# Kernel tuning notes

Hardware: AMD Instinct MI355X
Metric: run time of the kernel (lower is better)

The kernel has to match this reference:

```python
import jax, jax.numpy as jnp
import numpy as np

V, N = 3, 32768
C2, C3 = 256, 32          # feat_ch_2D, feat_ch_3D
H = W = 128               # 2D feature map size
D = 32                    # 3D volume feature size
CIN = C2 + C3             # 288, MLP in_channels


def setup_inputs() -> dict:
    key = jax.random.key(0)
    ks = jax.random.split(key, 16)
    sc = 0.02
    inp = {
        'pts': jax.random.uniform(ks[0], (1, N, 3), minval=-0.5, maxval=0.5),
        'pts_proj': jax.random.uniform(ks[1], (1, N, 2), minval=-1.0, maxval=1.0),
        'img_feat0': jax.random.normal(ks[2], (V, C2, H, W)),
        'img_feat1': jax.random.normal(ks[3], (V, C2, H, W)),
        'vol_feat0': jax.random.normal(ks[4], (V, C3, D, D, D)),
        'vol_feat1': jax.random.normal(ks[5], (V, C3, D, D, D)),
        'W0': jax.random.normal(ks[6], (1024, CIN)) * sc,  'b0': jnp.zeros((1024,)),
        'W1': jax.random.normal(ks[7], (512, CIN + 1024)) * sc, 'b1': jnp.zeros((512,)),
        'W2': jax.random.normal(ks[8], (256, CIN + 512)) * sc,  'b2': jnp.zeros((256,)),
        'W3': jax.random.normal(ks[9], (128, CIN + 256)) * sc,  'b3': jnp.zeros((128,)),
        'W4': jax.random.normal(ks[10], (1, 128)) * sc,         'b4': jnp.zeros((1,)),
        'mean_num': 3,
    }
    return inp


def _gs2d(feat, gx, gy):
    # feat: [C,H,W]; gx,gy: [N] normalized coords in [-1,1]
    C, Hh, Ww = feat.shape
    ix = jnp.clip(((gx + 1.0) * Ww - 1.0) * 0.5, 0.0, Ww - 1.0)  # align_corners=False, border pad
    iy = jnp.clip(((gy + 1.0) * Hh - 1.0) * 0.5, 0.0, Hh - 1.0)
    x0f, y0f = jnp.floor(ix), jnp.floor(iy)
    wx, wy = ix - x0f, iy - y0f
    x0 = x0f.astype(jnp.int32); x1 = jnp.minimum(x0 + 1, Ww - 1)
    y0 = y0f.astype(jnp.int32); y1 = jnp.minimum(y0 + 1, Hh - 1)
    v00 = feat[:, y0, x0]; v01 = feat[:, y0, x1]
    v10 = feat[:, y1, x0]; v11 = feat[:, y1, x1]
    return (v00 * (1 - wy) * (1 - wx) + v01 * (1 - wy) * wx
            + v10 * wy * (1 - wx) + v11 * wy * wx)  # [C,N]


def _gs3d(feat, gx, gy, gz):
    # feat: [C,D,H,W]; grid x->W, y->H, z->D (torch grid_sample convention)
    C, Dd, Hh, Ww = feat.shape
    ix = jnp.clip(((gx + 1.0) * Ww - 1.0) * 0.5, 0.0, Ww - 1.0)
    iy = jnp.clip(((gy + 1.0) * Hh - 1.0) * 0.5, 0.0, Hh - 1.0)
    iz = jnp.clip(((gz + 1.0) * Dd - 1.0) * 0.5, 0.0, Dd - 1.0)
    x0f, y0f, z0f = jnp.floor(ix), jnp.floor(iy), jnp.floor(iz)
    wx, wy, wz = ix - x0f, iy - y0f, iz - z0f
    x0 = x0f.astype(jnp.int32); x1 = jnp.minimum(x0 + 1, Ww - 1)
    y0 = y0f.astype(jnp.int32); y1 = jnp.minimum(y0 + 1, Hh - 1)
    z0 = z0f.astype(jnp.int32); z1 = jnp.minimum(z0 + 1, Dd - 1)
    def g(zi, yi, xi):
        return feat[:, zi, yi, xi]  # [C,N]
    out = (g(z0, y0, x0) * (1 - wz) * (1 - wy) * (1 - wx)
           + g(z0, y0, x1) * (1 - wz) * (1 - wy) * wx
           + g(z0, y1, x0) * (1 - wz) * wy * (1 - wx)
           + g(z0, y1, x1) * (1 - wz) * wy * wx
           + g(z1, y0, x0) * wz * (1 - wy) * (1 - wx)
           + g(z1, y0, x1) * wz * (1 - wy) * wx
           + g(z1, y1, x0) * wz * wy * (1 - wx)
           + g(z1, y1, x1) * wz * wy * wx)
    return out  # [C,N]


def _lrelu(x):
    return jnp.where(x >= 0, x, 0.2 * x)


def _conv1x1(Wm, bm, x):
    # x: [V,C,N] -> [V,O,N]
    return jnp.einsum('oc,vcn->von', Wm, x) + bm[None, :, None]


def _mlp0(x, W0, b0, W1, b1, W2, b2, W3, b3):
    out = _lrelu(_conv1x1(W0, b0, x))
    out = _lrelu(_conv1x1(W1, b1, jnp.concatenate([x, out], axis=1)))
    out = _lrelu(_conv1x1(W2, b2, jnp.concatenate([x, out], axis=1)))
    out = _lrelu(_conv1x1(W3, b3, jnp.concatenate([x, out], axis=1)))
    return out  # [V,128,N]


def _forward(pts, pts_proj, img_feats, vol_feats,
             W0, b0, W1, b1, W2, b2, W3, b3, W4, b4, mean_num):
    v = img_feats[0].shape[0]
    gx2 = jnp.broadcast_to(pts_proj[:, :, 0], (v, pts_proj.shape[1]))
    gy2 = jnp.broadcast_to(pts_proj[:, :, 1], (v, pts_proj.shape[1]))
    p = pts * 2.0  # pts *= 2.0 before 3D sampling
    gx3 = jnp.broadcast_to(p[:, :, 0], (v, p.shape[1]))
    gy3 = jnp.broadcast_to(p[:, :, 1], (v, p.shape[1]))
    gz3 = jnp.broadcast_to(p[:, :, 2], (v, p.shape[1]))
    outs = []
    for img_feat, vol_feat in zip(img_feats, vol_feats):
        f2 = jax.vmap(_gs2d)(img_feat, gx2, gy2)            # [V,C2,N]
        f3 = jax.vmap(_gs3d)(vol_feat, gx3, gy3, gz3)       # [V,C3,N]
        pt_feat = jnp.concatenate([f2, f3], axis=1)         # [V,288,N]
        pt_out0 = _mlp0(pt_feat, W0, b0, W1, b1, W2, b2, W3, b3)
        pt_out0_mean = jnp.mean(pt_out0[:mean_num], axis=0, keepdims=True)  # [1,128,N]
        sdf = jax.nn.sigmoid(_conv1x1(W4, b4, pt_out0_mean))                # [1,1,N]
        outs.append(jnp.transpose(sdf, (0, 2, 1)))                          # [1,N,1]
    return tuple(outs)


def reference(pts, pts_proj, img_feat0, img_feat1, vol_feat0, vol_feat1,
              W0, b0, W1, b1, W2, b2, W3, b3, W4, b4, mean_num):
    return _forward(pts, pts_proj, [img_feat0, img_feat1], [vol_feat0, vol_feat1],
                    W0, b0, W1, b1, W2, b2, W3, b3, W4, b4, mean_num)
```

## Files before the change

### kernel.cpp

```cpp
#include <hip/hip_runtime.h>
#include <hip/hip_bf16.h>

#define NV 3
#define NPTS 32768
#define C2C 256
#define C3C 32
#define CINC 288
#define CINP 320
#define HH 128
#define WWW 128
#define DDD 32

typedef short bh8 __attribute__((ext_vector_type(8)));
typedef float fx4 __attribute__((ext_vector_type(4)));
typedef unsigned short us4 __attribute__((ext_vector_type(4)));

__device__ __forceinline__ float b2f(unsigned short u) {
    unsigned int x = ((unsigned int)u) << 16;
    return __uint_as_float(x);
}
__device__ __forceinline__ unsigned short f2b(float f) {
    unsigned int x = __float_as_uint(f);
    unsigned int r = (x + 0x7FFFu + ((x >> 16) & 1u)) >> 16;
    return (unsigned short)r;
}

__device__ __forceinline__ void gl2lds16(const unsigned short* g, unsigned short* l) {
    __builtin_amdgcn_global_load_lds(
        (const __attribute__((address_space(1))) unsigned int*)g,
        (__attribute__((address_space(3))) unsigned int*)l, 16, 0, 0);
}

__device__ __forceinline__ int xcd_swz(int orig, int nwg) {
    int xcd = orig & 7;
    int q = nwg >> 3, r = nwg & 7;
    int base = (xcd < r) ? xcd * (q + 1) : r * (q + 1) + (xcd - r) * q;
    return base + (orig >> 3);
}

__global__ void k_wpad4(const float* __restrict__ s0, const float* __restrict__ s1,
                        const float* __restrict__ s2, const float* __restrict__ s3,
                        unsigned short* __restrict__ d0, unsigned short* __restrict__ d1,
                        unsigned short* __restrict__ d2, unsigned short* __restrict__ d3) {
    const int Ms[4] = {1024, 512, 256, 128};
    const int Kps[4] = {320, 1344, 832, 576};
    int i = blockIdx.y;
    int M = Ms[i], Kp = Kps[i];
    int idx = blockIdx.x * 256 + threadIdx.x;
    if (idx >= M * Kp) return;
    const float* src = (i == 0) ? s0 : (i == 1) ? s1 : (i == 2) ? s2 : s3;
    unsigned short* dst = (i == 0) ? d0 : (i == 1) ? d1 : (i == 2) ? d2 : d3;
    int m = idx / Kp, k = idx - m * Kp;
    int Ksrc = Kp - 32;
    float v;
    if (k < CINC) v = src[(size_t)m * Ksrc + k];
    else if (k < CINP) v = 0.0f;
    else v = src[(size_t)m * Ksrc + (k - 32)];
    dst[idx] = f2b(v);
}

__global__ void k_timg(const float* __restrict__ in0, const float* __restrict__ in1,
                       unsigned short* __restrict__ out, size_t lvlStride) {
    int lvl = blockIdx.z >> 2, cb = blockIdx.z & 3;
    const float* in = lvl ? in1 : in0;
    int v = blockIdx.x >> 7, y = blockIdx.x & 127;
    int x0 = blockIdx.y << 6, c0 = cb << 6;
    __shared__ float t[64][65];
    int tx = threadIdx.x & 63, tg = threadIdx.x >> 6;
    const float* src = in + (((size_t)(v * C2C + c0) * HH + y) * WWW + x0);
#pragma unroll
    for (int i = 0; i < 16; i++) {
        int cl = tg * 16 + i;
        t[cl][tx] = src[(size_t)cl * (HH * WWW) + tx];
    }
    __syncthreads();
    unsigned short* dst = out + lvl * lvlStride + ((size_t)(v * HH + y) * WWW + x0) * C2C + c0;
#pragma unroll
    for (int i = 0; i < 16; i++) {
        int xl = tg * 16 + i;
        dst[(size_t)xl * C2C + tx] = f2b(t[tx][xl]);
    }
}

__global__ void k_tvol(const float* __restrict__ in0, const float* __restrict__ in1,
                       unsigned short* __restrict__ out, size_t lvlStride) {
    int lvl = blockIdx.z;
    const float* in = lvl ? in1 : in0;
    int v = blockIdx.x;
    int s0 = blockIdx.y << 8;
    __shared__ float t[32][257];
    int tid = threadIdx.x;
    const float* src = in + (size_t)v * C3C * 32768 + s0;
#pragma unroll
    for (int c = 0; c < 32; c++) t[c][tid] = src[(size_t)c * 32768 + tid];
    __syncthreads();
    unsigned short* dst = out + lvl * lvlStride + ((size_t)v * 32768 + s0) * C3C;
    int c = tid & 31, sb = tid >> 5;
#pragma unroll
    for (int j = 0; j < 32; j++) {
        int sl = j * 8 + sb;
        dst[(size_t)sl * C3C + c] = f2b(t[c][sl]);
    }
}

__global__ __launch_bounds__(256) void k_sample(const float* __restrict__ pts, const float* __restrict__ proj,
                         const unsigned short* __restrict__ imgT, const unsigned short* __restrict__ volT,
                         unsigned short* __restrict__ ptT, int n0, int Nk) {
    int w = threadIdx.x >> 6, l = threadIdx.x & 63;
    int i = blockIdx.x * 4 + w;
    int v = blockIdx.y;
    int n = n0 + i;
    unsigned short* dstRow = ptT + (size_t)(v * Nk + i) * CINP;

    {
        float gx = proj[n * 2 + 0], gy = proj[n * 2 + 1];
        float ix = fminf(fmaxf(((gx + 1.0f) * (float)WWW - 1.0f) * 0.5f, 0.0f), (float)(WWW - 1));
        float iy = fminf(fmaxf(((gy + 1.0f) * (float)HH - 1.0f) * 0.5f, 0.0f), (float)(HH - 1));
        float x0f = floorf(ix), y0f = floorf(iy);
        float wx = ix - x0f, wy = iy - y0f;
        int x0 = (int)x0f, y0 = (int)y0f;
        int x1 = min(x0 + 1, WWW - 1), y1 = min(y0 + 1, HH - 1);
        const unsigned short* base = imgT + (size_t)v * HH * WWW * C2C;
        us4 a = *((const us4*)(base + ((size_t)(y0 * WWW + x0)) * C2C) + l);
        us4 b = *((const us4*)(base + ((size_t)(y0 * WWW + x1)) * C2C) + l);
        us4 c = *((const us4*)(base + ((size_t)(y1 * WWW + x0)) * C2C) + l);
        us4 d = *((const us4*)(base + ((size_t)(y1 * WWW + x1)) * C2C) + l);
        float w00 = (1.0f - wy) * (1.0f - wx), w01 = (1.0f - wy) * wx;
        float w10 = wy * (1.0f - wx), w11 = wy * wx;
        us4 rv;
#pragma unroll
        for (int r = 0; r < 4; r++) {
            float f = b2f(a[r]) * w00 + b2f(b[r]) * w01 + b2f(c[r]) * w10 + b2f(d[r]) * w11;
            rv[r] = f2b(f);
        }
        *(us4*)(dstRow + l * 4) = rv;
    }
    {
        float gx = pts[n * 3 + 0] * 2.0f, gy = pts[n * 3 + 1] * 2.0f, gz = pts[n * 3 + 2] * 2.0f;
        float ix = fminf(fmaxf(((gx + 1.0f) * (float)DDD - 1.0f) * 0.5f, 0.0f), (float)(DDD - 1));
        float iy = fminf(fmaxf(((gy + 1.0f) * (float)DDD - 1.0f) * 0.5f, 0.0f), (float)(DDD - 1));
        float iz = fminf(fmaxf(((gz + 1.0f) * (float)DDD - 1.0f) * 0.5f, 0.0f), (float)(DDD - 1));
        float x0f = floorf(ix), y0f = floorf(iy), z0f = floorf(iz);
        float wx = ix - x0f, wy = iy - y0f, wz = iz - z0f;
        int x0 = (int)x0f, y0 = (int)y0f, z0 = (int)z0f;
        int x1 = min(x0 + 1, DDD - 1), y1 = min(y0 + 1, DDD - 1), z1 = min(z0 + 1, DDD - 1);
        int c = l & 31, zs = l >> 5;
        int zi = zs ? z1 : z0;
        float wzs = zs ? wz : (1.0f - wz);
        const unsigned short* base = volT + (size_t)v * 32768 * C3C;
        float f00 = b2f(base[((size_t)((zi * 32 + y0) * 32 + x0)) * C3C + c]);
        float f01 = b2f(base[((size_t)((zi * 32 + y0) * 32 + x1)) * C3C + c]);
        float f10 = b2f(base[((size_t)((zi * 32 + y1) * 32 + x0)) * C3C + c]);
        float f11 = b2f(base[((size_t)((zi * 32 + y1) * 32 + x1)) * C3C + c]);
        float r = (f00 * (1.0f - wy) * (1.0f - wx) + f01 * (1.0f - wy) * wx +
                   f10 * wy * (1.0f - wx) + f11 * wy * wx) * wzs;
        float other = __shfl_xor(r, 32);
        r += other;
        if (zs == 0) dstRow[C2C + c] = f2b(r);
    }
    if (l < 8) *(us4*)(dstRow + CINC + l * 4) = (us4){0, 0, 0, 0};
}

template <int K2, int M>
__device__ __forceinline__ void gemm128_body(const unsigned short* __restrict__ A,
                                             const unsigned short* __restrict__ B1,
                                             const unsigned short* __restrict__ B2,
                                             const float* __restrict__ bias,
                                             unsigned short* __restrict__ C) {
    constexpr int K1 = CINP;
    constexpr int K = K1 + K2;
    constexpr int nt1 = K1 / 32;
    constexpr int nt = K / 32;
    __shared__ unsigned short Ash[2][128 * 32];
    __shared__ unsigned short Bsh[2][128 * 32];
    int tid = threadIdx.x;
    int w = tid >> 6, l = tid & 63;
    int la = l & 15, lg = l >> 4;
    int wm = w & 1, wn = w >> 1;
    int gx = gridDim.x;
    int nwg = gx * gridDim.y;
    int bid = xcd_swz(blockIdx.y * gx + blockIdx.x, nwg);
    int mBlk = (bid % gx) * 128;
    int nBlk = (bid / gx) * 128;
    int sRow = l >> 2, sCol = (l & 3) * 8;
    int r0 = w * 32 + sRow, r1 = r0 + 16;

    const unsigned short* Ag = A + (size_t)mBlk * K;
    const unsigned short* B1g = B1 + (size_t)nBlk * K1;
    const unsigned short* B2g = (K2 > 0) ? (B2 + (size_t)nBlk * K2) : (const unsigned short*)0;

    fx4 acc[4][4];
#pragma unroll
    for (int mi = 0; mi < 4; mi++)
#pragma unroll
        for (int ni = 0; ni < 4; ni++) acc[mi][ni] = (fx4){0.f, 0.f, 0.f, 0.f};

    auto stage = [&](int t, int nxt) {
        const unsigned short* as = Ag + t * 32 + sCol;
        gl2lds16(as + (size_t)r0 * K, &Ash[nxt][r0 * 32 + sCol]);
        gl2lds16(as + (size_t)r1 * K, &Ash[nxt][r1 * 32 + sCol]);
        const unsigned short* bs;
        size_t ldb;
        if (t < nt1) { bs = B1g + t * 32 + sCol; ldb = (size_t)K1; }
        else         { bs = B2g + (t - nt1) * 32 + sCol; ldb = (size_t)K2; }
        gl2lds16(bs + (size_t)r0 * ldb, &Bsh[nxt][r0 * 32 + sCol]);
        gl2lds16(bs + (size_t)r1 * ldb, &Bsh[nxt][r1 * 32 + sCol]);
    };

    stage(0, 0);
    asm volatile("s_waitcnt vmcnt(0)" ::: "memory");
    __builtin_amdgcn_s_barrier();
    for (int t = 0; t < nt; t++) {
        int cur = t & 1;
        if (t + 1 < nt) stage(t + 1, cur ^ 1);
        bh8 af[4], bfv[4];
#pragma unroll
        for (int mi = 0; mi < 4; mi++) af[mi] = *(const bh8*)&Ash[cur][(wm * 64 + mi * 16 + la) * 32 + lg * 8];
#pragma unroll
        for (int ni = 0; ni < 4; ni++) bfv[ni] = *(const bh8*)&Bsh[cur][(wn * 64 + ni * 16 + la) * 32 + lg * 8];
#pragma unroll
        for (int mi = 0; mi < 4; mi++)
#pragma unroll
            for (int ni = 0; ni < 4; ni++)
                acc[mi][ni] = __builtin_amdgcn_mfma_f32_16x16x32_bf16(af[mi], bfv[ni], acc[mi][ni], 0, 0, 0);
        asm volatile("s_waitcnt lgkmcnt(0)" ::: "memory");
        if (t + 1 < nt) asm volatile("s_waitcnt vmcnt(0)" ::: "memory");
        __builtin_amdgcn_s_barrier();
    }

#pragma unroll
    for (int mi = 0; mi < 4; mi++) {
        int m0 = mBlk + wm * 64 + mi * 16 + lg * 4;
        fx4 bb = *(const fx4*)(bias + m0);
#pragma unroll
        for (int ni = 0; ni < 4; ni++) {
            int n = nBlk + wn * 64 + ni * 16 + la;
            us4 rv;
#pragma unroll
            for (int r = 0; r < 4; r++) {
                float x = acc[mi][ni][r] + bb[r];
                x = (x >= 0.0f) ? x : 0.2f * x;
                rv[r] = f2b(x);
            }
            *(us4*)(C + (size_t)n * M + m0) = rv;
        }
    }
}

__global__ __launch_bounds__(256) void k_g0(const unsigned short* __restrict__ A, const unsigned short* __restrict__ B1,
                                            const float* __restrict__ bias, unsigned short* __restrict__ C) {
    gemm128_body<0, 1024>(A, B1, nullptr, bias, C);
}
__global__ __launch_bounds__(256) void k_g2(const unsigned short* __restrict__ A, const unsigned short* __restrict__ B1,
                                            const unsigned short* __restrict__ B2, const float* __restrict__ bias,
                                            unsigned short* __restrict__ C) {
    gemm128_body<512, 256>(A, B1, B2, bias, C);
}
__global__ __launch_bounds__(256) void k_g3(const unsigned short* __restrict__ A, const unsigned short* __restrict__ B1,
                                            const unsigned short* __restrict__ B2, const float* __restrict__ bias,
                                            unsigned short* __restrict__ C) {
    gemm128_body<256, 128>(A, B1, B2, bias, C);
}

__global__ __launch_bounds__(512) void k_g1(const unsigned short* __restrict__ A,
                                            const unsigned short* __restrict__ B1,
                                            const unsigned short* __restrict__ B2,
                                            const float* __restrict__ bias,
                                            unsigned short* __restrict__ C) {
    constexpr int Kp = 1344;
    constexpr int K2 = 1024;
    constexpr int M = 512;
    constexpr int nt = Kp >> 6;
    __shared__ unsigned short As[2][256 * 64];
    __shared__ unsigned short Bs[2][256 * 64];
    int tid = threadIdx.x;
    int w = tid >> 6, l = tid & 63;
    int la = l & 15, lg = l >> 4;
    int wm = w >> 2, wn = w & 3;
    int gx = gridDim.x;
    int nwg = gx * gridDim.y;
    int bid = xcd_swz(blockIdx.y * gx + blockIdx.x, nwg);
    int mBlk = (bid % gx) * 256;
    int nBlk = (bid / gx) * 256;

    const unsigned short* Ag = A + (size_t)mBlk * Kp;

    fx4 acc[8][4];
#pragma unroll
    for (int mi = 0; mi < 8; mi++)
#pragma unroll
        for (int ni = 0; ni < 4; ni++) acc[mi][ni] = (fx4){0.f, 0.f, 0.f, 0.f};

    auto stageB = [&](int t, int nxt) {
        const unsigned short* bsrc;
        size_t ldb;
        int kc;
        if (t < 5) { bsrc = B1; ldb = CINP; kc = t * 64; }
        else       { bsrc = B2; ldb = (size_t)K2; kc = (t - 5) * 64; }
        bsrc += (size_t)nBlk * ldb + kc;
#pragma unroll
        for (int h = 0; h < 2; h++)
#pragma unroll
            for (int j = 0; j < 2; j++) {
                int idx = j * 512 + tid;
                int r = (h << 7) + (idx >> 3);
                int c = (idx & 7) ^ (r & 7);
                gl2lds16(bsrc + (size_t)r * ldb + c * 8, &Bs[nxt][(h << 13) + idx * 8]);
            }
    };
    auto stageA1 = [&](int t, int nxt) {
        const unsigned short* asrc = Ag + t * 64;
#pragma unroll
        for (int h = 0; h < 2; h++) {
            int idx = tid;
            int r = (h << 7) + (idx >> 3);
            int c = (idx & 7) ^ (r & 7);
            gl2lds16(asrc + (size_t)r * Kp + c * 8, &As[nxt][(h << 13) + idx * 8]);
        }
    };
    auto stageA2 = [&](int t, int nxt) {
        const unsigned short* asrc = Ag + t * 64;
#pragma unroll
        for (int h = 0; h < 2; h++) {
            int idx = 512 + tid;
            int r = (h << 7) + (idx >> 3);
            int c = (idx & 7) ^ (r & 7);
            gl2lds16(asrc + (size_t)r * Kp + c * 8, &As[nxt][(h << 13) + idx * 8]);
        }
    };

    stageB(0, 0);
    stageA1(0, 0);
    stageA2(0, 0);
    asm volatile("s_waitcnt vmcnt(0)" ::: "memory");
    __builtin_amdgcn_s_barrier();

    for (int t = 0; t < nt; t++) {
        int cur = t & 1;
        const unsigned short* Ab = &As[cur][0];
        const unsigned short* Bb = &Bs[cur][0];
        bh8 afr[4][2];
#pragma unroll
        for (int p = 0; p < 4; p++) {
            int qm = p >> 1, qn = p & 1;
            if (qn == 0) {
#pragma unroll
                for (int m2 = 0; m2 < 4; m2++)
#pragma unroll
                    for (int s = 0; s < 2; s++) {
                        int row = wm * 128 + (qm * 4 + m2) * 16 + la;
                        int c = (s * 4 + lg) ^ (row & 7);
                        afr[m2][s] = *(const bh8*)&Ab[row * 64 + c * 8];
                    }
            }
            bh8 bfr[2][2];
#pragma unroll
            for (int n2 = 0; n2 < 2; n2++)
#pragma unroll
                for (int s = 0; s < 2; s++) {
                    int row = wn * 64 + (qn * 2 + n2) * 16 + la;
                    int c = (s * 4 + lg) ^ (row & 7);
                    bfr[n2][s] = *(const bh8*)&Bb[row * 64 + c * 8];
                }
            if (p == 0 && t + 1 < nt) stageB(t + 1, cur ^ 1);
            if (p == 1 && t + 1 < nt) stageA1(t + 1, cur ^ 1);
            if (p == 2 && t + 1 < nt) stageA2(t + 1, cur ^ 1);
            __builtin_amdgcn_s_barrier();
            __builtin_amdgcn_s_setprio(1);
#pragma unroll
            for (int m2 = 0; m2 < 4; m2++)
#pragma unroll
                for (int n2 = 0; n2 < 2; n2++)
#pragma unroll
                    for (int s = 0; s < 2; s++)
                        acc[qm * 4 + m2][qn * 2 + n2] = __builtin_amdgcn_mfma_f32_16x16x32_bf16(
                            afr[m2][s], bfr[n2][s], acc[qm * 4 + m2][qn * 2 + n2], 0, 0, 0);
            __builtin_amdgcn_s_setprio(0);
            if (p == 1) {
                if (t + 1 < nt) asm volatile("s_waitcnt vmcnt(6)" ::: "memory");
                else            asm volatile("s_waitcnt vmcnt(0)" ::: "memory");
            }
            if (p == 3) {
                asm volatile("s_waitcnt lgkmcnt(0)" ::: "memory");
                if (t + 1 < nt) asm volatile("s_waitcnt vmcnt(2)" ::: "memory");
            }
            __builtin_amdgcn_s_barrier();
        }
    }

#pragma unroll
    for (int mi = 0; mi < 8; mi++) {
        int m0 = mBlk + wm * 128 + mi * 16 + lg * 4;
        fx4 bb = *(const fx4*)(bias + m0);
#pragma unroll
        for (int ni = 0; ni < 4; ni++) {
            int n = nBlk + wn * 64 + ni * 16 + la;
            us4 rv;
#pragma unroll
            for (int r = 0; r < 4; r++) {
                float x = acc[mi][ni][r] + bb[r];
                x = (x >= 0.0f) ? x : 0.2f * x;
                rv[r] = f2b(x);
            }
            *(us4*)(C + (size_t)n * M + m0) = rv;
        }
    }
}

__global__ __launch_bounds__(256) void k_head(const unsigned short* __restrict__ o3, const float* __restrict__ W4,
                       const float* __restrict__ b4, const int* __restrict__ mn_p,
                       float* __restrict__ out, int n0, int Nk, int level) {
    int wv = threadIdx.x >> 6, l = threadIdx.x & 63;
    int sub = l >> 4, cl = l & 15;
    int i = blockIdx.x * 16 + wv * 4 + sub;
    if (i >= Nk) return;
    int mn = *mn_p;
    if (mn > NV) mn = NV;
    if (mn < 1) mn = 1;
    fx4 w0 = *(const fx4*)(W4 + cl * 8);
    fx4 w1 = *(const fx4*)(W4 + cl * 8 + 4);
    float s = 0.0f;
    for (int v = 0; v < mn; v++) {
        bh8 x = *(const bh8*)(o3 + (size_t)(v * Nk + i) * 128 + cl * 8);
#pragma unroll
        for (int r = 0; r < 4; r++) s += w0[r] * b2f((unsigned short)x[r]);
#pragma unroll
        for (int r = 0; r < 4; r++) s += w1[r] * b2f((unsigned short)x[4 + r]);
    }
#pragma unroll
    for (int m = 1; m < 16; m <<= 1) s += __shfl_xor(s, m);
    if (cl == 0) {
        s = s / (float)mn + b4[0];
        out[(size_t)level * NPTS + n0 + i] = 1.0f / (1.0f + expf(-s));
    }
}

extern "C" void kernel_launch(void* const* d_in, const int* in_sizes, int n_in,
                              void* d_out, int out_size, void* d_ws, size_t ws_size,
                              hipStream_t stream) {
    const float* pts = (const float*)d_in[0];
    const float* proj = (const float*)d_in[1];
    const float* img[2] = {(const float*)d_in[2], (const float*)d_in[3]};
    const float* vol[2] = {(const float*)d_in[4], (const float*)d_in[5]};
    const float* Wf[4] = {(const float*)d_in[6], (const float*)d_in[8], (const float*)d_in[10], (const float*)d_in[12]};
    const float* bf[4] = {(const float*)d_in[7], (const float*)d_in[9], (const float*)d_in[11], (const float*)d_in[13]};
    const float* W4 = (const float*)d_in[14];
    const float* b4 = (const float*)d_in[15];
    const int* mn = (const int*)d_in[16];
    float* out = (float*)d_out;

    const int Kp[4] = {320, 1344, 832, 576};
    const int Msz[4] = {1024, 512, 256, 128};

    char* ws = (char*)d_ws;
    size_t off = 0;
    auto alloc = [&](size_t bytes) -> char* {
        char* p = ws + off;
        off = (off + bytes + 255) & ~(size_t)255;
        return p;
    };

    const size_t imgStride = (size_t)NV * HH * WWW * C2C;
    const size_t volStride = (size_t)NV * 32768 * C3C;

    unsigned short* Wb[4];
    for (int i = 0; i < 4; i++) Wb[i] = (unsigned short*)alloc((size_t)Msz[i] * Kp[i] * 2);
    unsigned short* imgT = (unsigned short*)alloc(2 * imgStride * 2);
    unsigned short* volT = (unsigned short*)alloc(2 * volStride * 2);
    size_t fixed = off;

    const size_t perPt = (size_t)NV * 2 * (CINP + 1024 + 512);
    int Nk = NPTS;
    if (fixed + (size_t)Nk * perPt + 4096 > ws_size) {
        size_t avail = (ws_size > fixed + 4096) ? (ws_size - fixed - 4096) : 0;
        long nk = (long)(avail / perPt);
        nk = (nk / 512) * 512;
        if (nk < 512) nk = 512;
        if (nk > NPTS) nk = NPTS;
        Nk = (int)nk;
    }
    unsigned short* ptT = (unsigned short*)alloc((size_t)NV * Nk * CINP * 2);
    unsigned short* o0 = (unsigned short*)alloc((size_t)NV * Nk * 1024 * 2);
    unsigned short* o1 = (unsigned short*)alloc((size_t)NV * Nk * 512 * 2);
    unsigned short* o2 = o0;
    unsigned short* o3 = o0 + (size_t)NV * Nk * 256;

    k_wpad4<<<dim3(2688, 4), 256, 0, stream>>>(Wf[0], Wf[1], Wf[2], Wf[3], Wb[0], Wb[1], Wb[2], Wb[3]);
    k_timg<<<dim3(NV * HH, WWW / 64, 8), 256, 0, stream>>>(img[0], img[1], imgT, imgStride);
    k_tvol<<<dim3(NV, 32768 / 256, 2), 256, 0, stream>>>(vol[0], vol[1], volT, volStride);

    for (int lvl = 0; lvl < 2; lvl++) {
        for (int n0 = 0; n0 < NPTS; n0 += Nk) {
            int nk = NPTS - n0 < Nk ? NPTS - n0 : Nk;
            int NC = NV * nk;
            k_sample<<<dim3(nk / 4, NV), 256, 0, stream>>>(pts, proj, imgT + lvl * imgStride,
                                                           volT + lvl * volStride, ptT, n0, nk);
            k_g0<<<dim3(1024 / 128, NC / 128), 256, 0, stream>>>(Wb[0], ptT, bf[0], o0);
            k_g1<<<dim3(512 / 256, NC / 256), 512, 0, stream>>>(Wb[1], ptT, o0, bf[1], o1);
            k_g2<<<dim3(256 / 128, NC / 128), 256, 0, stream>>>(Wb[2], ptT, o1, bf[2], o2);
            k_g3<<<dim3(128 / 128, NC / 128), 256, 0, stream>>>(Wb[3], ptT, o2, bf[3], o3);
            k_head<<<(nk + 15) / 16, 256, 0, stream>>>(o3, W4, b4, mn, out, n0, nk, lvl);
        }
    }
}
```

Measured before the change: 1.065 ms.

## Triple-buffer GEMM LDS staging and duplicate kernels per pyramid level

Switches the shared GEMM body from double to triple buffering in LDS, so tile t+2 is in flight while tile t is computed, using partial vmcnt waits. It also splits each kernel into per-level copies and reorders the launch loop so both levels run inside each chunk. The extra buffer is meant to hide more global-load latency, at the cost of more LDS per block, which may reduce occupancy. The duplicated kernels likely only change naming for profiling or scheduling and add code size.

```diff
diff --git a/kernel.cpp b/kernel.cpp
--- a/kernel.cpp
+++ b/kernel.cpp
@@ -103,7 +103,7 @@
     }
 }
 
-__global__ __launch_bounds__(256) void k_sample(const float* __restrict__ pts, const float* __restrict__ proj,
+__device__ __forceinline__ void sample_body(const float* __restrict__ pts, const float* __restrict__ proj,
                          const unsigned short* __restrict__ imgT, const unsigned short* __restrict__ volT,
                          unsigned short* __restrict__ ptT, int n0, int Nk) {
     int w = threadIdx.x >> 6, l = threadIdx.x & 63;
@@ -161,6 +161,15 @@
     if (l < 8) *(us4*)(dstRow + CINC + l * 4) = (us4){0, 0, 0, 0};
 }
 
+__global__ __launch_bounds__(256) void k_sampleL0(const float* p, const float* pr, const unsigned short* im,
+                                                  const unsigned short* vo, unsigned short* pt, int n0, int Nk) {
+    sample_body(p, pr, im, vo, pt, n0, Nk);
+}
+__global__ __launch_bounds__(256) void k_sampleL1(const float* p, const float* pr, const unsigned short* im,
+                                                  const unsigned short* vo, unsigned short* pt, int n0, int Nk) {
+    sample_body(p, pr, im, vo, pt, n0, Nk);
+}
+
 template <int K2, int M>
 __device__ __forceinline__ void gemm128_body(const unsigned short* __restrict__ A,
                                              const unsigned short* __restrict__ B1,
@@ -171,8 +180,8 @@
     constexpr int K = K1 + K2;
     constexpr int nt1 = K1 / 32;
     constexpr int nt = K / 32;
-    __shared__ unsigned short Ash[2][128 * 32];
-    __shared__ unsigned short Bsh[2][128 * 32];
+    __shared__ unsigned short Ash[3][128 * 32];
+    __shared__ unsigned short Bsh[3][128 * 32];
     int tid = threadIdx.x;
     int w = tid >> 6, l = tid & 63;
     int la = l & 15, lg = l >> 4;
@@ -195,24 +204,25 @@
 #pragma unroll
         for (int ni = 0; ni < 4; ni++) acc[mi][ni] = (fx4){0.f, 0.f, 0.f, 0.f};
 
-    auto stage = [&](int t, int nxt) {
+    auto stage = [&](int t, int b) {
         const unsigned short* as = Ag + t * 32 + sCol;
-        gl2lds16(as + (size_t)r0 * K, &Ash[nxt][r0 * 32 + sCol]);
-        gl2lds16(as + (size_t)r1 * K, &Ash[nxt][r1 * 32 + sCol]);
+        gl2lds16(as + (size_t)r0 * K, &Ash[b][r0 * 32 + sCol]);
+        gl2lds16(as + (size_t)r1 * K, &Ash[b][r1 * 32 + sCol]);
         const unsigned short* bs;
         size_t ldb;
         if (t < nt1) { bs = B1g + t * 32 + sCol; ldb = (size_t)K1; }
         else         { bs = B2g + (t - nt1) * 32 + sCol; ldb = (size_t)K2; }
-        gl2lds16(bs + (size_t)r0 * ldb, &Bsh[nxt][r0 * 32 + sCol]);
-        gl2lds16(bs + (size_t)r1 * ldb, &Bsh[nxt][r1 * 32 + sCol]);
+        gl2lds16(bs + (size_t)r0 * ldb, &Bsh[b][r0 * 32 + sCol]);
+        gl2lds16(bs + (size_t)r1 * ldb, &Bsh[b][r1 * 32 + sCol]);
     };
 
     stage(0, 0);
-    asm volatile("s_waitcnt vmcnt(0)" ::: "memory");
+    if (nt > 1) stage(1, 1);
+    asm volatile("s_waitcnt vmcnt(4)" ::: "memory");
     __builtin_amdgcn_s_barrier();
+    int cur = 0, nxt2 = 2;
     for (int t = 0; t < nt; t++) {
-        int cur = t & 1;
-        if (t + 1 < nt) stage(t + 1, cur ^ 1);
+        if (t + 2 < nt) stage(t + 2, nxt2);
         bh8 af[4], bfv[4];
 #pragma unroll
         for (int mi = 0; mi < 4; mi++) af[mi] = *(const bh8*)&Ash[cur][(wm * 64 + mi * 16 + la) * 32 + lg * 8];
@@ -224,8 +234,11 @@
             for (int ni = 0; ni < 4; ni++)
                 acc[mi][ni] = __builtin_amdgcn_mfma_f32_16x16x32_bf16(af[mi], bfv[ni], acc[mi][ni], 0, 0, 0);
         asm volatile("s_waitcnt lgkmcnt(0)" ::: "memory");
-        if (t + 1 < nt) asm volatile("s_waitcnt vmcnt(0)" ::: "memory");
+        if (t + 2 < nt)      asm volatile("s_waitcnt vmcnt(4)" ::: "memory");
+        else if (t + 1 < nt) asm volatile("s_waitcnt vmcnt(0)" ::: "memory");
         __builtin_amdgcn_s_barrier();
+        cur = (cur == 2) ? 0 : cur + 1;
+        nxt2 = (nxt2 == 2) ? 0 : nxt2 + 1;
     }
 
 #pragma unroll
@@ -247,26 +260,24 @@
     }
 }
 
-__global__ __launch_bounds__(256) void k_g0(const unsigned short* __restrict__ A, const unsigned short* __restrict__ B1,
-                                            const float* __restrict__ bias, unsigned short* __restrict__ C) {
-    gemm128_body<0, 1024>(A, B1, nullptr, bias, C);
-}
-__global__ __launch_bounds__(256) void k_g2(const unsigned short* __restrict__ A, const unsigned short* __restrict__ B1,
-                                            const unsigned short* __restrict__ B2, const float* __restrict__ bias,
-                                            unsigned short* __restrict__ C) {
-    gemm128_body<512, 256>(A, B1, B2, bias, C);
-}
-__global__ __launch_bounds__(256) void k_g3(const unsigned short* __restrict__ A, const unsigned short* __restrict__ B1,
-                                            const unsigned short* __restrict__ B2, const float* __restrict__ bias,
-                                            unsigned short* __restrict__ C) {
-    gemm128_body<256, 128>(A, B1, B2, bias, C);
-}
-
-__global__ __launch_bounds__(512) void k_g1(const unsigned short* __restrict__ A,
-                                            const unsigned short* __restrict__ B1,
-                                            const unsigned short* __restrict__ B2,
-                                            const float* __restrict__ bias,
-                                            unsigned short* __restrict__ C) {
+__global__ __launch_bounds__(256) void k_g0L0(const unsigned short* A, const unsigned short* B1,
+                                              const float* b, unsigned short* C) { gemm128_body<0, 1024>(A, B1, nullptr, b, C); }
+__global__ __launch_bounds__(256) void k_g0L1(const unsigned short* A, const unsigned short* B1,
+                                              const float* b, unsigned short* C) { gemm128_body<0, 1024>(A, B1, nullptr, b, C); }
+__global__ __launch_bounds__(256) void k_g2L0(const unsigned short* A, const unsigned short* B1, const unsigned short* B2,
+                                              const float* b, unsigned short* C) { gemm128_body<512, 256>(A, B1, B2, b, C); }
+__global__ __launch_bounds__(256) void k_g2L1(const unsigned short* A, const unsigned short* B1, const unsigned short* B2,
+                                              const float* b, unsigned short* C) { gemm128_body<512, 256>(A, B1, B2, b, C); }
+__global__ __launch_bounds__(256) void k_g3L0(const unsigned short* A, const unsigned short* B1, const unsigned short* B2,
+                                              const float* b, unsigned short* C) { gemm128_body<256, 128>(A, B1, B2, b, C); }
+__global__ __launch_bounds__(256) void k_g3L1(const unsigned short* A, const unsigned short* B1, const unsigned short* B2,
+                                              const float* b, unsigned short* C) { gemm128_body<256, 128>(A, B1, B2, b, C); }
+
+__device__ __forceinline__ void g1_body(const unsigned short* __restrict__ A,
+                                        const unsigned short* __restrict__ B1,
+                                        const unsigned short* __restrict__ B2,
+                                        const float* __restrict__ bias,
+                                        unsigned short* __restrict__ C) {
     constexpr int Kp = 1344;
     constexpr int K2 = 1024;
     constexpr int M = 512;
@@ -407,7 +418,12 @@
     }
 }
 
-__global__ __launch_bounds__(256) void k_head(const unsigned short* __restrict__ o3, const float* __restrict__ W4,
+__global__ __launch_bounds__(512) void k_g1L0(const unsigned short* A, const unsigned short* B1, const unsigned short* B2,
+                                              const float* b, unsigned short* C) { g1_body(A, B1, B2, b, C); }
+__global__ __launch_bounds__(512) void k_g1L1(const unsigned short* A, const unsigned short* B1, const unsigned short* B2,
+                                              const float* b, unsigned short* C) { g1_body(A, B1, B2, b, C); }
+
+__device__ __forceinline__ void head_body(const unsigned short* __restrict__ o3, const float* __restrict__ W4,
                        const float* __restrict__ b4, const int* __restrict__ mn_p,
                        float* __restrict__ out, int n0, int Nk, int level) {
     int wv = threadIdx.x >> 6, l = threadIdx.x & 63;
@@ -435,6 +451,15 @@
     }
 }
 
+__global__ __launch_bounds__(256) void k_headL0(const unsigned short* o3, const float* W4, const float* b4,
+                                                const int* mn, float* out, int n0, int Nk) {
+    head_body(o3, W4, b4, mn, out, n0, Nk, 0);
+}
+__global__ __launch_bounds__(256) void k_headL1(const unsigned short* o3, const float* W4, const float* b4,
+                                                const int* mn, float* out, int n0, int Nk) {
+    head_body(o3, W4, b4, mn, out, n0, Nk, 1);
+}
+
 extern "C" void kernel_launch(void* const* d_in, const int* in_sizes, int n_in,
                               void* d_out, int out_size, void* d_ws, size_t ws_size,
                               hipStream_t stream) {
@@ -489,17 +514,20 @@
     k_timg<<<dim3(NV * HH, WWW / 64, 8), 256, 0, stream>>>(img[0], img[1], imgT, imgStride);
     k_tvol<<<dim3(NV, 32768 / 256, 2), 256, 0, stream>>>(vol[0], vol[1], volT, volStride);
 
-    for (int lvl = 0; lvl < 2; lvl++) {
-        for (int n0 = 0; n0 < NPTS; n0 += Nk) {
-            int nk = NPTS - n0 < Nk ? NPTS - n0 : Nk;
-            int NC = NV * nk;
-            k_sample<<<dim3(nk / 4, NV), 256, 0, stream>>>(pts, proj, imgT + lvl * imgStride,
-                                                           volT + lvl * volStride, ptT, n0, nk);
-            k_g0<<<dim3(1024 / 128, NC / 128), 256, 0, stream>>>(Wb[0], ptT, bf[0], o0);
-            k_g1<<<dim3(512 / 256, NC / 256), 512, 0, stream>>>(Wb[1], ptT, o0, bf[1], o1);
-            k_g2<<<dim3(256 / 128, NC / 128), 256, 0, stream>>>(Wb[2], ptT, o1, bf[2], o2);
-            k_g3<<<dim3(128 / 128, NC / 128), 256, 0, stream>>>(Wb[3], ptT, o2, bf[3], o3);
-            k_head<<<(nk + 15) / 16, 256, 0, stream>>>(o3, W4, b4, mn, out, n0, nk, lvl);
-        }
-    }
-}
+    for (int n0 = 0; n0 < NPTS; n0 += Nk) {
+        int nk = NPTS - n0 < Nk ? NPTS - n0 : Nk;
+        int NC = NV * nk;
+        k_sampleL0<<<dim3(nk / 4, NV), 256, 0, stream>>>(pts, proj, imgT, volT, ptT, n0, nk);
+        k_g0L0<<<dim3(1024 / 128, NC / 128), 256, 0, stream>>>(Wb[0], ptT, bf[0], o0);
+        k_g1L0<<<dim3(512 / 256, NC / 256), 512, 0, stream>>>(Wb[1], ptT, o0, bf[1], o1);
+        k_g2L0<<<dim3(256 / 128, NC / 128), 256, 0, stream>>>(Wb[2], ptT, o1, bf[2], o2);
+        k_g3L0<<<dim3(128 / 128, NC / 128), 256, 0, stream>>>(Wb[3], ptT, o2, bf[3], o3);
+        k_headL0<<<(nk + 15) / 16, 256, 0, stream>>>(o3, W4, b4, mn, out, n0, nk);
+        k_sampleL1<<<dim3(nk / 4, NV), 256, 0, stream>>>(pts, proj, imgT + imgStride, volT + volStride, ptT, n0, nk);
+        k_g0L1<<<dim3(1024 / 128, NC / 128), 256, 0, stream>>>(Wb[0], ptT, bf[0], o0);
+        k_g1L1<<<dim3(512 / 256, NC / 256), 512, 0, stream>>>(Wb[1], ptT, o0, bf[1], o1);
+        k_g2L1<<<dim3(256 / 128, NC / 128), 256, 0, stream>>>(Wb[2], ptT, o1, bf[2], o2);
+        k_g3L1<<<dim3(128 / 128, NC / 128), 256, 0, stream>>>(Wb[3], ptT, o2, bf[3], o3);
+        k_headL1<<<(nk + 15) / 16, 256, 0, stream>>>(o3, W4, b4, mn, out, n0, nk);
+    }
+}
```

Measured after the change: 1.059 ms. Within noise of the previous version (-0.6%).
